# Performance work log

Measured on AMD Instinct MI355X. Metric: run time of the kernel, lower is better.

## Reference

```python
import jax, jax.numpy as jnp
import numpy as np

# tinygemm asymmetric int4 convention
QUANT_MIN, QUANT_MAX = 0, 15
MID_POINT = (QUANT_MAX + QUANT_MIN + 1) / 2.0  # 8.0
OUT_F, IN_F, GROUP = 8192, 8192, 128
M_TOKENS = 64


def setup_inputs() -> dict:
    key = jax.random.key(0)
    kx, kw = jax.random.split(key)
    x = jax.random.normal(kx, (M_TOKENS, IN_F), dtype=jnp.float32)
    # Materialize quantized params exactly as quantize_weight_tinygemm does.
    w = jax.random.normal(kw, (OUT_F, IN_F), dtype=jnp.float32) * 0.02
    ng = IN_F // GROUP
    wg = w.reshape(OUT_F, ng, GROUP)
    min_val = wg.min(axis=2)
    max_val = wg.max(axis=2)
    scale = jnp.maximum((max_val - min_val) / float(QUANT_MAX - QUANT_MIN), 1.1920929e-7)
    zero_point = min_val + scale * MID_POINT
    min_val_recon = zero_point - scale * MID_POINT
    q = jnp.clip(jnp.round((wg - min_val_recon[..., None]) / scale[..., None]),
                 QUANT_MIN, QUANT_MAX).astype(jnp.int32)
    int_data = q.reshape(OUT_F, IN_F)  # values in [0, 15]
    # tinygemm layout: (n_groups, out_features, 2) with [..., 0]=scale, [..., 1]=zero_point
    scale_and_zero = jnp.stack([scale, zero_point], axis=-1).transpose(1, 0, 2)
    return {"x": x, "int_data": int_data, "scale_and_zero": scale_and_zero}


def reference(x, int_data, scale_and_zero):
    # Dequant: w = (q - MID_POINT) * scale + zero_point, per group of GROUP along in_features.
    ng = IN_F // GROUP
    q = int_data.reshape(OUT_F, ng, GROUP).astype(x.dtype)
    scale = scale_and_zero[..., 0].T[:, :, None]       # (OUT_F, ng, 1)
    zero_point = scale_and_zero[..., 1].T[:, :, None]  # (OUT_F, ng, 1)
    w = ((q - MID_POINT) * scale + zero_point).reshape(OUT_F, IN_F)
    return x @ w.T  # (M, OUT_F)
```

## Files before the change

### kernel.cpp

```cpp
#include <hip/hip_runtime.h>
#include <hip/hip_bf16.h>


#define OUT_F 8192
#define IN_F  8192
#define M_TOK 64
#define GROUP 128
#define BN    64
#define KSPLIT 4
#define KR    (IN_F / KSPLIT)
#define GROUPS (KR / GROUP)

typedef short short8 __attribute__((ext_vector_type(8)));
typedef float f32x4  __attribute__((ext_vector_type(4)));

__device__ __forceinline__ unsigned pk(float lo, float hi) {
    __hip_bfloat162 h = __float22bfloat162_rn(float2{lo, hi});
    unsigned r;
    __builtin_memcpy(&r, &h, sizeof(r));
    return r;
}

__global__ void zero_out(float* __restrict__ p) {
    const int i = (blockIdx.x * 256 + threadIdx.x) * 4;
    *(float4*)(p + i) = float4{0.f, 0.f, 0.f, 0.f};
}

__global__ __launch_bounds__(512, 4)
void woq_gemm(const float* __restrict__ x,
              const int*   __restrict__ qw,
              const float* __restrict__ sz,
              float*       __restrict__ outp) {
    __shared__ int lds_x[2][4096];
    __shared__ int lds_w[2][4096];

    const int t    = threadIdx.x;
    const int lane = t & 63;
    const int wv   = t >> 6;
    const int wn   = wv & 3;
    const int kh   = wv >> 2;
    const int n0   = blockIdx.x * BN;
    const int k0   = blockIdx.y * KR;

    const int nlo  = lane & 15;
    const int quad = lane >> 4;
    const int row  = wn * 16 + nlo;
    const int n1   = n0 + row;

    const int tr = t >> 5;
    const int kc = t & 31;

    f32x4 acc[4];
#pragma unroll
    for (int mi = 0; mi < 4; ++mi) acc[mi] = (f32x4){0.f, 0.f, 0.f, 0.f};

    int4   wq[4];
    float2 sc[4];
    float4 xs[4];

    auto stage_load = [&](int g) {
        const int kg = k0 + g * GROUP;
#pragma unroll
        for (int i = 0; i < 4; ++i) {
            const int r = i * 16 + tr;
            wq[i] = *(const int4*)(qw + (size_t)(n0 + r) * IN_F + kg + kc * 4);
        }
        const int gg = kg >> 7;
#pragma unroll
        for (int i = 0; i < 4; ++i) {
            const int r = i * 16 + tr;
            sc[i] = *(const float2*)(sz + ((size_t)gg * OUT_F + n0 + r) * 2);
        }
#pragma unroll
        for (int j = 0; j < 2; ++j) {
            const int slot  = t + 512 * j;
            const int chunk = slot >> 6;
            const int l     = slot & 63;
            const int m     = ((chunk & 3) << 4) + (l & 15);
            const int kk    = ((chunk >> 2) << 5) + ((l >> 4) << 3);
            const float4* p = (const float4*)(x + (size_t)m * IN_F + kg + kk);
            xs[2 * j]     = p[0];
            xs[2 * j + 1] = p[1];
        }
    };

    auto stage_write = [&](int buf) {
        int* wb = lds_w[buf];
#pragma unroll
        for (int i = 0; i < 4; ++i) {
            const int r = i * 16 + tr;
            const float s = sc[i].x;
            const float c = fmaf(-8.f, sc[i].x, sc[i].y);
            int2 v;
            v.x = (int)pk(fmaf((float)wq[i].x, s, c), fmaf((float)wq[i].y, s, c));
            v.y = (int)pk(fmaf((float)wq[i].z, s, c), fmaf((float)wq[i].w, s, c));
            const int idx = (r * 64 + kc * 2) ^ ((r & 7) << 2);
            *(int2*)&wb[idx] = v;
        }
        int* xb = lds_x[buf];
#pragma unroll
        for (int j = 0; j < 2; ++j) {
            const int slot = t + 512 * j;
            int4 bv;
            bv.x = (int)pk(xs[2 * j].x,     xs[2 * j].y);
            bv.y = (int)pk(xs[2 * j].z,     xs[2 * j].w);
            bv.z = (int)pk(xs[2 * j + 1].x, xs[2 * j + 1].y);
            bv.w = (int)pk(xs[2 * j + 1].z, xs[2 * j + 1].w);
            *(int4*)&xb[slot * 4] = bv;
        }
    };

    stage_load(0);
    stage_write(0);
    __syncthreads();

    for (int g = 0; g < GROUPS; ++g) {
        if (g + 1 < GROUPS) stage_load(g + 1);

        const int* xb = lds_x[g & 1];
        const int* wb = lds_w[g & 1];
#pragma unroll
        for (int s = 0; s < 2; ++s) {
            const int ks = kh * 2 + s;
            const int bidx = (row * 64 + ks * 16 + quad * 4) ^ ((row & 7) << 2);
            const short8 b = *(const short8*)&wb[bidx];
            short8 a[4];
#pragma unroll
            for (int mi = 0; mi < 4; ++mi)
                a[mi] = *(const short8*)&xb[((ks * 4 + mi) * 64 + lane) * 4];
#pragma unroll
            for (int mi = 0; mi < 4; ++mi)
                acc[mi] = __builtin_amdgcn_mfma_f32_16x16x32_bf16(a[mi], b, acc[mi], 0, 0, 0);
        }

        if (g + 1 < GROUPS) {
            stage_write((g + 1) & 1);
            __syncthreads();
        }
    }

    __syncthreads();
    f32x4* redp = (f32x4*)&lds_x[0][0];
    if (kh == 1) {
#pragma unroll
        for (int mi = 0; mi < 4; ++mi)
            redp[(wn * 4 + mi) * 64 + lane] = acc[mi];
    }
    __syncthreads();
    if (kh == 0) {
#pragma unroll
        for (int mi = 0; mi < 4; ++mi)
            acc[mi] += redp[(wn * 4 + mi) * 64 + lane];
#pragma unroll
        for (int mi = 0; mi < 4; ++mi)
#pragma unroll
            for (int r = 0; r < 4; ++r)
                atomicAdd(outp + (size_t)(mi * 16 + quad * 4 + r) * OUT_F + n1, acc[mi][r]);
    }
}

extern "C" void kernel_launch(void* const* d_in, const int* in_sizes, int n_in,
                              void* d_out, int out_size, void* d_ws, size_t ws_size,
                              hipStream_t stream) {
    const float* x  = (const float*)d_in[0];
    const int*   qw = (const int*)d_in[1];
    const float* sz = (const float*)d_in[2];
    float* out = (float*)d_out;

    zero_out<<<dim3((M_TOK * OUT_F) / (256 * 4)), 256, 0, stream>>>(out);
    woq_gemm<<<dim3(OUT_F / BN, KSPLIT), 512, 0, stream>>>(x, qw, sz, out);
}
```

Measured before the change: 376.3 us.

## Replace split-K with full-K blocks of 32 columns and in-block reduction

Drops the zeroing kernel and split-K atomics. Each block now owns 32 output columns over the whole K range, stepping 512 wide, and reduces its eight waves' partial sums in shared memory before plain stores. Weight LDS layout changes to the MFMA operand order, and each wave issues two B fragments per step. Risks are a grid of only 256 blocks, larger LDS per block (lower occupancy), and an extra barrier each step.

```diff
diff --git a/kernel.cpp b/kernel.cpp
--- a/kernel.cpp
+++ b/kernel.cpp
@@ -5,11 +5,9 @@
 #define OUT_F 8192
 #define IN_F  8192
 #define M_TOK 64
-#define GROUP 128
-#define BN    64
-#define KSPLIT 4
-#define KR    (IN_F / KSPLIT)
-#define GROUPS (KR / GROUP)
+#define BN    32
+#define KSTEP 512
+#define NSTEP (IN_F / KSTEP)
 
 typedef short short8 __attribute__((ext_vector_type(8)));
 typedef float f32x4  __attribute__((ext_vector_type(4)));
@@ -21,141 +19,140 @@
     return r;
 }
 
-__global__ void zero_out(float* __restrict__ p) {
-    const int i = (blockIdx.x * 256 + threadIdx.x) * 4;
-    *(float4*)(p + i) = float4{0.f, 0.f, 0.f, 0.f};
-}
-
-__global__ __launch_bounds__(512, 4)
+__global__ __launch_bounds__(512, 2)
 void woq_gemm(const float* __restrict__ x,
               const int*   __restrict__ qw,
               const float* __restrict__ sz,
               float*       __restrict__ outp) {
-    __shared__ int lds_x[2][4096];
-    __shared__ int lds_w[2][4096];
+    __shared__ int lds_w[2][8192];
+    __shared__ int lds_x[16384];
 
     const int t    = threadIdx.x;
     const int lane = t & 63;
     const int wv   = t >> 6;
-    const int wn   = wv & 3;
-    const int kh   = wv >> 2;
-    const int n0   = blockIdx.x * BN;
-    const int k0   = blockIdx.y * KR;
-
     const int nlo  = lane & 15;
     const int quad = lane >> 4;
-    const int row  = wn * 16 + nlo;
-    const int n1   = n0 + row;
+    const int n0   = blockIdx.x * BN;
 
-    const int tr = t >> 5;
-    const int kc = t & 31;
+    int4   wq[8];
+    float2 sc[8];
+    float4 xv[8][2];
 
-    f32x4 acc[4];
+    auto load_x = [&](int kb) {
 #pragma unroll
-    for (int mi = 0; mi < 4; ++mi) acc[mi] = (f32x4){0.f, 0.f, 0.f, 0.f};
-
-    int4   wq[4];
-    float2 sc[4];
-    float4 xs[4];
-
-    auto stage_load = [&](int g) {
-        const int kg = k0 + g * GROUP;
-#pragma unroll
-        for (int i = 0; i < 4; ++i) {
-            const int r = i * 16 + tr;
-            wq[i] = *(const int4*)(qw + (size_t)(n0 + r) * IN_F + kg + kc * 4);
-        }
-        const int gg = kg >> 7;
-#pragma unroll
-        for (int i = 0; i < 4; ++i) {
-            const int r = i * 16 + tr;
-            sc[i] = *(const float2*)(sz + ((size_t)gg * OUT_F + n0 + r) * 2);
-        }
-#pragma unroll
-        for (int j = 0; j < 2; ++j) {
+        for (int j = 0; j < 8; ++j) {
             const int slot  = t + 512 * j;
             const int chunk = slot >> 6;
             const int l     = slot & 63;
             const int m     = ((chunk & 3) << 4) + (l & 15);
             const int kk    = ((chunk >> 2) << 5) + ((l >> 4) << 3);
-            const float4* p = (const float4*)(x + (size_t)m * IN_F + kg + kk);
-            xs[2 * j]     = p[0];
-            xs[2 * j + 1] = p[1];
+            const float4* p = (const float4*)(x + (size_t)m * IN_F + kb * KSTEP + kk);
+            xv[j][0] = p[0];
+            xv[j][1] = p[1];
         }
     };
-
-    auto stage_write = [&](int buf) {
+    auto load_s = [&](int kb) {
+#pragma unroll
+        for (int i = 0; i < 8; ++i) {
+            const int r  = wv * 4 + (i >> 1);
+            const int gg = kb * 4 + (i & 1) * 2 + (lane >> 5);
+            sc[i] = *(const float2*)(sz + ((size_t)gg * OUT_F + n0 + r) * 2);
+        }
+    };
+    auto load_w = [&](int kb) {
+#pragma unroll
+        for (int i = 0; i < 8; ++i) {
+            const int r    = wv * 4 + (i >> 1);
+            const int koff = (i & 1) * 256 + lane * 4;
+            wq[i] = *(const int4*)(qw + (size_t)(n0 + r) * IN_F + kb * KSTEP + koff);
+        }
+    };
+    auto write_x = [&]() {
+#pragma unroll
+        for (int j = 0; j < 8; ++j) {
+            const int slot = t + 512 * j;
+            int4 v;
+            v.x = (int)pk(xv[j][0].x, xv[j][0].y);
+            v.y = (int)pk(xv[j][0].z, xv[j][0].w);
+            v.z = (int)pk(xv[j][1].x, xv[j][1].y);
+            v.w = (int)pk(xv[j][1].z, xv[j][1].w);
+            *(int4*)&lds_x[slot * 4] = v;
+        }
+    };
+    auto write_w = [&](int buf) {
         int* wb = lds_w[buf];
 #pragma unroll
-        for (int i = 0; i < 4; ++i) {
-            const int r = i * 16 + tr;
+        for (int i = 0; i < 8; ++i) {
+            const int r    = wv * 4 + (i >> 1);
+            const int koff = (i & 1) * 256 + lane * 4;
             const float s = sc[i].x;
             const float c = fmaf(-8.f, sc[i].x, sc[i].y);
             int2 v;
             v.x = (int)pk(fmaf((float)wq[i].x, s, c), fmaf((float)wq[i].y, s, c));
             v.y = (int)pk(fmaf((float)wq[i].z, s, c), fmaf((float)wq[i].w, s, c));
-            const int idx = (r * 64 + kc * 2) ^ ((r & 7) << 2);
+            const int chunk = (koff >> 5) * 2 + (r >> 4);
+            const int ll    = (r & 15) + ((koff >> 3) & 3) * 16;
+            const int idx   = (chunk * 64 + ll) * 4 + ((koff & 4) >> 1);
             *(int2*)&wb[idx] = v;
-        }
-        int* xb = lds_x[buf];
-#pragma unroll
-        for (int j = 0; j < 2; ++j) {
-            const int slot = t + 512 * j;
-            int4 bv;
-            bv.x = (int)pk(xs[2 * j].x,     xs[2 * j].y);
-            bv.y = (int)pk(xs[2 * j].z,     xs[2 * j].w);
-            bv.z = (int)pk(xs[2 * j + 1].x, xs[2 * j + 1].y);
-            bv.w = (int)pk(xs[2 * j + 1].z, xs[2 * j + 1].w);
-            *(int4*)&xb[slot * 4] = bv;
         }
     };
 
-    stage_load(0);
-    stage_write(0);
+    f32x4 acc[4][2];
+#pragma unroll
+    for (int mi = 0; mi < 4; ++mi)
+#pragma unroll
+        for (int nj = 0; nj < 2; ++nj)
+            acc[mi][nj] = (f32x4){0.f, 0.f, 0.f, 0.f};
+
+    load_x(0); load_s(0); load_w(0);
+    write_x(); write_w(0);
     __syncthreads();
 
-    for (int g = 0; g < GROUPS; ++g) {
-        if (g + 1 < GROUPS) stage_load(g + 1);
+    for (int kb = 0; kb < NSTEP; ++kb) {
+        if (kb + 1 < NSTEP) { load_x(kb + 1); load_s(kb + 1); load_w(kb + 1); }
 
-        const int* xb = lds_x[g & 1];
-        const int* wb = lds_w[g & 1];
+        const int* wb = lds_w[kb & 1];
 #pragma unroll
-        for (int s = 0; s < 2; ++s) {
-            const int ks = kh * 2 + s;
-            const int bidx = (row * 64 + ks * 16 + quad * 4) ^ ((row & 7) << 2);
-            const short8 b = *(const short8*)&wb[bidx];
+        for (int s2 = 0; s2 < 2; ++s2) {
+            const int ks = wv * 2 + s2;
+            short8 b0 = *(const short8*)&wb[((ks * 2 + 0) * 64 + lane) * 4];
+            short8 b1 = *(const short8*)&wb[((ks * 2 + 1) * 64 + lane) * 4];
             short8 a[4];
 #pragma unroll
             for (int mi = 0; mi < 4; ++mi)
-                a[mi] = *(const short8*)&xb[((ks * 4 + mi) * 64 + lane) * 4];
+                a[mi] = *(const short8*)&lds_x[((ks * 4 + mi) * 64 + lane) * 4];
 #pragma unroll
-            for (int mi = 0; mi < 4; ++mi)
-                acc[mi] = __builtin_amdgcn_mfma_f32_16x16x32_bf16(a[mi], b, acc[mi], 0, 0, 0);
+            for (int mi = 0; mi < 4; ++mi) {
+                acc[mi][0] = __builtin_amdgcn_mfma_f32_16x16x32_bf16(a[mi], b0, acc[mi][0], 0, 0, 0);
+                acc[mi][1] = __builtin_amdgcn_mfma_f32_16x16x32_bf16(a[mi], b1, acc[mi][1], 0, 0, 0);
+            }
         }
+        __syncthreads();
 
-        if (g + 1 < GROUPS) {
-            stage_write((g + 1) & 1);
+        if (kb + 1 < NSTEP) {
+            write_x();
+            write_w((kb + 1) & 1);
             __syncthreads();
         }
     }
 
+    f32x4* red = (f32x4*)lds_x;
+#pragma unroll
+    for (int mi = 0; mi < 4; ++mi)
+#pragma unroll
+        for (int nj = 0; nj < 2; ++nj)
+            red[(wv * 8 + mi * 2 + nj) * 64 + lane] = acc[mi][nj];
     __syncthreads();
-    f32x4* redp = (f32x4*)&lds_x[0][0];
-    if (kh == 1) {
+    {
+        const int fi = wv;
+        const int mi = fi >> 1, nj = fi & 1;
+        f32x4 s = red[(0 * 8 + fi) * 64 + lane];
 #pragma unroll
-        for (int mi = 0; mi < 4; ++mi)
-            redp[(wn * 4 + mi) * 64 + lane] = acc[mi];
-    }
-    __syncthreads();
-    if (kh == 0) {
+        for (int w2 = 1; w2 < 8; ++w2)
+            s += red[(w2 * 8 + fi) * 64 + lane];
 #pragma unroll
-        for (int mi = 0; mi < 4; ++mi)
-            acc[mi] += redp[(wn * 4 + mi) * 64 + lane];
-#pragma unroll
-        for (int mi = 0; mi < 4; ++mi)
-#pragma unroll
-            for (int r = 0; r < 4; ++r)
-                atomicAdd(outp + (size_t)(mi * 16 + quad * 4 + r) * OUT_F + n1, acc[mi][r]);
+        for (int r = 0; r < 4; ++r)
+            outp[(size_t)(mi * 16 + quad * 4 + r) * OUT_F + n0 + nj * 16 + nlo] = s[r];
     }
 }
 
@@ -165,8 +162,5 @@
     const float* x  = (const float*)d_in[0];
     const int*   qw = (const int*)d_in[1];
     const float* sz = (const float*)d_in[2];
-    float* out = (float*)d_out;
-
-    zero_out<<<dim3((M_TOK * OUT_F) / (256 * 4)), 256, 0, stream>>>(out);
-    woq_gemm<<<dim3(OUT_F / BN, KSPLIT), 512, 0, stream>>>(x, qw, sz, out);
+    woq_gemm<<<dim3(OUT_F / BN), 512, 0, stream>>>(x, qw, sz, (float*)d_out);
 }
```

Result: slower. 400.5 us (+6.4%).
